# Performance work log

Measured on AMD Instinct MI355X. Metric: run time of the kernel, lower is better.

The kernel has to match this reference:

```python
import jax, jax.numpy as jnp
import numpy as np

D_MODEL = 4096
N_Q_HEAD = 32
N_KV_HEAD = 8
HEAD_DIM = D_MODEL // N_Q_HEAD  # 128
N_REP = N_Q_HEAD // N_KV_HEAD   # 4
B, T = 2, 2048


def _rope_tables(seq_len, head_dim, dtype=jnp.float32):
    # theta_i = 10000^(-2*(i-1)/d) for i=1..d/2  (matches torch.pow(10000, -2*(arange(1,d/2+1)-1)/d))
    i = jnp.arange(head_dim // 2, dtype=dtype)
    theta = jnp.power(10000.0, -2.0 * i / head_dim)
    angles = jnp.outer(jnp.arange(seq_len, dtype=dtype), theta)  # [T, d/2]
    return jnp.cos(angles), jnp.sin(angles)


def _apply_rope(x, cos, sin):
    # x: [B, T, h, HD]; pairs are consecutive elements (view_as_complex semantics)
    B_, T_, h, hd = x.shape
    xp = x.reshape(B_, T_, h, hd // 2, 2)
    xr, xi = xp[..., 0], xp[..., 1]
    c = cos[None, :T_, None, :]
    s = sin[None, :T_, None, :]
    out_r = xr * c - xi * s
    out_i = xr * s + xi * c
    return jnp.stack([out_r, out_i], axis=-1).reshape(B_, T_, h, hd)


def setup_inputs() -> dict:
    key = jax.random.key(0)
    ks = jax.random.split(key, 5)
    scale = 0.02
    x = jax.random.normal(ks[0], (B, T, D_MODEL), dtype=jnp.float32)
    wq = jax.random.normal(ks[1], (D_MODEL, N_Q_HEAD * HEAD_DIM), dtype=jnp.float32) * scale
    wk = jax.random.normal(ks[2], (D_MODEL, N_KV_HEAD * HEAD_DIM), dtype=jnp.float32) * scale
    wv = jax.random.normal(ks[3], (D_MODEL, N_KV_HEAD * HEAD_DIM), dtype=jnp.float32) * scale
    wo = jax.random.normal(ks[4], (N_Q_HEAD * HEAD_DIM, D_MODEL), dtype=jnp.float32) * scale
    # causal mask: 1 where masked (strict upper triangle), per masked_fill(mask==1, -inf)
    attention_mask = jnp.triu(jnp.ones((T, T), dtype=jnp.int32), k=1)
    return {"x": x, "wq": wq, "wk": wk, "wv": wv, "wo": wo, "attention_mask": attention_mask}


def reference(x, wq, wk, wv, wo, attention_mask):
    B_, T_, _ = x.shape
    xq = (x @ wq).reshape(B_, T_, N_Q_HEAD, HEAD_DIM)
    xk = (x @ wk).reshape(B_, T_, N_KV_HEAD, HEAD_DIM)
    xv = (x @ wv).reshape(B_, T_, N_KV_HEAD, HEAD_DIM)

    cos, sin = _rope_tables(T_, HEAD_DIM, x.dtype)
    xq = _apply_rope(xq, cos, sin)
    xk = _apply_rope(xk, cos, sin)

    # GQA: repeat kv heads (training path: no cache)
    xk = jnp.repeat(xk, N_REP, axis=2)  # [B, T, HQ, HD]
    xv = jnp.repeat(xv, N_REP, axis=2)

    q = xq.transpose(0, 2, 1, 3)  # [B, H, T, HD]
    k = xk.transpose(0, 2, 1, 3)
    v = xv.transpose(0, 2, 1, 3)

    scores = jnp.einsum('bhqd,bhkd->bhqk', q, k) / jnp.sqrt(jnp.asarray(HEAD_DIM, x.dtype))
    scores = jnp.where(attention_mask[None, None, :, :] == 1, -jnp.inf, scores)
    probs = jax.nn.softmax(scores, axis=-1)
    out = jnp.einsum('bhqk,bhkd->bhqd', probs, v)
    out = out.transpose(0, 2, 1, 3).reshape(B_, T_, N_Q_HEAD * HEAD_DIM)
    return out @ wo
```

## Files before the change

### kernel.cpp

```cpp
#include <hip/hip_runtime.h>
#include <hip/hip_bf16.h>
#include <math.h>

typedef __hip_bfloat16 bf16;
typedef short bf16x8 __attribute__((ext_vector_type(8)));
typedef float f32x4 __attribute__((ext_vector_type(4)));
typedef float f32x16 __attribute__((ext_vector_type(16)));
typedef unsigned int u32;
typedef unsigned short u16;

#define GLD16(g, l)                                                            \
  __builtin_amdgcn_global_load_lds(                                            \
      (const __attribute__((address_space(1))) void*)(g),                      \
      (__attribute__((address_space(3))) void*)(l), 16, 0, 0)

#define SBAR() __builtin_amdgcn_s_barrier()
#define VMCNT(n) asm volatile("s_waitcnt vmcnt(" #n ")")
#define LGKM0() asm volatile("s_waitcnt lgkmcnt(0)")

__global__ void convert_f32_bf16(const float* __restrict__ in,
                                 bf16* __restrict__ out) {
  size_t i = ((size_t)blockIdx.x * 256 + threadIdx.x) * 4;
  float4 v = *(const float4*)(in + i);
  out[i + 0] = __float2bfloat16(v.x);
  out[i + 1] = __float2bfloat16(v.y);
  out[i + 2] = __float2bfloat16(v.z);
  out[i + 3] = __float2bfloat16(v.w);
}

__global__ void transpose_f32_bf16(const float* __restrict__ in,
                                   bf16* __restrict__ out, int R, int C) {
  __shared__ bf16 tile[32][33];
  int tx = threadIdx.x & 31, ty = threadIdx.x >> 5;
  int c0 = blockIdx.x * 32, r0 = blockIdx.y * 32;
#pragma unroll
  for (int i = 0; i < 32; i += 8)
    tile[ty + i][tx] = __float2bfloat16(in[(size_t)(r0 + ty + i) * C + c0 + tx]);
  __syncthreads();
#pragma unroll
  for (int i = 0; i < 32; i += 8)
    out[(size_t)(c0 + ty + i) * R + r0 + tx] = tile[tx][ty + i];
}

__global__ void transpose_v(const bf16* __restrict__ V, bf16* __restrict__ VT) {
  __shared__ bf16 tile[32][33];
  int s = blockIdx.z, b = s >> 3, kvh = s & 7;
  int t0 = blockIdx.x * 32, d0 = blockIdx.y * 32;
  int tx = threadIdx.x & 31, ty = threadIdx.x >> 5;
#pragma unroll
  for (int i = 0; i < 32; i += 8)
    tile[ty + i][tx] =
        V[(size_t)(b * 2048 + t0 + ty + i) * 6144 + kvh * 128 + d0 + tx];
  __syncthreads();
#pragma unroll
  for (int i = 0; i < 32; i += 8)
    VT[((size_t)s * 128 + d0 + ty + i) * 2048 + t0 + tx] = tile[tx][ty + i];
}

__global__ void rope_table_k(float* __restrict__ tab) {
  int idx = blockIdx.x * 256 + threadIdx.x;
  int t = idx >> 6, i = idx & 63;
  float theta = powf(10000.0f, -2.0f * (float)i / 128.0f);
  float ang = (float)t * theta;
  tab[idx * 2 + 0] = cosf(ang);
  tab[idx * 2 + 1] = sinf(ang);
}

__global__ void rope_apply(bf16* __restrict__ X, const float* __restrict__ tab,
                           int nheads, int rowstride, float omul) {
  size_t idx = (size_t)blockIdx.x * 256 + threadIdx.x;
  int i = (int)(idx & 63);
  size_t rest = idx >> 6;
  int h = (int)(rest % nheads);
  size_t r = rest / nheads;
  int t = (int)(r & 2047);
  float c = tab[(t * 64 + i) * 2 + 0];
  float s = tab[(t * 64 + i) * 2 + 1];
  bf16* p = X + r * (size_t)rowstride + h * 128 + 2 * i;
  float xr = __bfloat162float(p[0]), xi = __bfloat162float(p[1]);
  p[0] = __float2bfloat16((xr * c - xi * s) * omul);
  p[1] = __float2bfloat16((xr * s + xi * c) * omul);
}

template <typename OutT>
__global__ __launch_bounds__(512, 2) void gemm_bt8(const bf16* __restrict__ A,
                                                   const bf16* __restrict__ BT,
                                                   OutT* __restrict__ C, int M,
                                                   int N, int K) {
  __shared__ bf16 AS[2][2][128 * 64];
  __shared__ bf16 BS[2][2][128 * 64];

  const int tid = threadIdx.x;
  const int lane = tid & 63;
  const int w = tid >> 6, wm = w >> 2, wn = w & 3;
  const int lr = lane & 15, hi = lane >> 4;

  int gx = gridDim.x;
  int nwg = gx * gridDim.y;
  int bid = blockIdx.y * gx + blockIdx.x;
  int swz = (bid & 7) * (nwg >> 3) + (bid >> 3);
  const int m0 = (swz / gx) * 256, n0 = (swz % gx) * 256;

  const int NKT = K >> 6;
  const int NI = K >> 7;
  const int srow = tid >> 3;
  const int scol = ((tid & 7) ^ (srow & 7)) << 3;

  f32x4 acc[8][4];
#pragma unroll
  for (int m = 0; m < 8; ++m)
#pragma unroll
    for (int n = 0; n < 4; ++n)
#pragma unroll
      for (int j = 0; j < 4; ++j) acc[m][n][j] = 0.f;

  auto STAGE_A = [&](int buf, int kt) {
    int kk0 = (kt < NKT) ? kt * 64 : 0;
#pragma unroll
    for (int hs = 0; hs < 4; ++hs) {
      int ha = hs >> 1, sa = hs & 1;
      const bf16* g = A + (size_t)(m0 + ha * 128 + sa * 64 + srow) * K + kk0 + scol;
      GLD16(g, &AS[buf][ha][(sa * 64 + srow) * 64 + (tid & 7) * 8]);
    }
  };
  auto STAGE_B = [&](int buf, int kt, int half) {
    int kk0 = (kt < NKT) ? kt * 64 : 0;
#pragma unroll
    for (int sa = 0; sa < 2; ++sa) {
      const bf16* g =
          BT + (size_t)(n0 + half * 128 + sa * 64 + srow) * K + kk0 + scol;
      GLD16(g, &BS[buf][half][(sa * 64 + srow) * 64 + (tid & 7) * 8]);
    }
  };

  bf16x8 bfr[4][2], afA[2][2], afB[2][2];
  auto READ_B = [&](int buf) {
#pragma unroll
    for (int n = 0; n < 4; ++n) {
      int row = (wn & 1) * 64 + n * 16 + lr;
#pragma unroll
      for (int kk = 0; kk < 2; ++kk)
        bfr[n][kk] = *(const bf16x8*)(&BS[buf][wn >> 1]
                                         [row * 64 + (((kk * 4 + hi) ^ (row & 7)) << 3)]);
    }
  };
  auto READ_A_TO = [&](bf16x8(&dst)[2][2], int buf, int q) {
#pragma unroll
    for (int mm = 0; mm < 2; ++mm) {
      int row = (q * 2 + mm) * 16 + lr;
#pragma unroll
      for (int kk = 0; kk < 2; ++kk)
        dst[mm][kk] = *(const bf16x8*)(&AS[buf][wm]
                                          [row * 64 + (((kk * 4 + hi) ^ (row & 7)) << 3)]);
    }
  };

#define MFMA16(q, AF)                                                          \
  do {                                                                         \
    _Pragma("unroll") for (int mm = 0; mm < 2; ++mm)                           \
        _Pragma("unroll") for (int n = 0; n < 4; ++n)                          \
        _Pragma("unroll") for (int kk = 0; kk < 2; ++kk)                       \
            acc[(q) * 2 + mm][n] = __builtin_amdgcn_mfma_f32_16x16x32_bf16(    \
                AF[mm][kk], bfr[n][kk], acc[(q) * 2 + mm][n], 0, 0, 0);        \
  } while (0)

  STAGE_A(0, 0);
  STAGE_B(0, 0, 0); STAGE_B(0, 0, 1);
  STAGE_B(1, 1, 0); STAGE_B(1, 1, 1);
  VMCNT(4);
  SBAR();

  for (int i = 0; i < NI; ++i) {
    int t = 2 * i;
    READ_B(0); READ_A_TO(afA, 0, 0); READ_A_TO(afB, 0, 1);
    STAGE_A(1, t + 1);
    SBAR(); LGKM0();
    __builtin_amdgcn_s_setprio(1); MFMA16(0, afA); MFMA16(1, afB);
    __builtin_amdgcn_s_setprio(0);
    SBAR();
    READ_A_TO(afA, 0, 2); READ_A_TO(afB, 0, 3);
    STAGE_B(0, t + 2, 0); STAGE_B(0, t + 2, 1);
    SBAR(); LGKM0();
    __builtin_amdgcn_s_setprio(1); MFMA16(2, afA); MFMA16(3, afB);
    __builtin_amdgcn_s_setprio(0);
    VMCNT(4);
    SBAR();
    READ_B(1); READ_A_TO(afA, 1, 0); READ_A_TO(afB, 1, 1);
    STAGE_A(0, t + 2);
    SBAR(); LGKM0();
    __builtin_amdgcn_s_setprio(1); MFMA16(0, afA); MFMA16(1, afB);
    __builtin_amdgcn_s_setprio(0);
    SBAR();
    READ_A_TO(afA, 1, 2); READ_A_TO(afB, 1, 3);
    STAGE_B(1, t + 3, 0); STAGE_B(1, t + 3, 1);
    SBAR(); LGKM0();
    __builtin_amdgcn_s_setprio(1); MFMA16(2, afA); MFMA16(3, afB);
    __builtin_amdgcn_s_setprio(0);
    VMCNT(4);
    SBAR();
  }

  VMCNT(0);
  SBAR();

#pragma unroll
  for (int m = 0; m < 8; ++m) {
    int row_base = m0 + wm * 128 + m * 16 + hi * 4;
#pragma unroll
    for (int n = 0; n < 4; ++n) {
      int col = n0 + wn * 64 + n * 16 + lr;
#pragma unroll
      for (int j = 0; j < 4; ++j) {
        float v = acc[m][n][j];
        if constexpr (sizeof(OutT) == 2)
          C[(size_t)(row_base + j) * N + col] = (OutT)__float2bfloat16(v);
        else
          C[(size_t)(row_base + j) * N + col] = (OutT)v;
      }
    }
  }
#undef MFMA16
}

static __device__ inline u32 cvtpk_bf16(float a, float b) {
  u32 r;
  asm("v_cvt_pk_bf16_f32 %0, %1, %2" : "=v"(r) : "v"(a), "v"(b));
  return r;
}

__global__ __launch_bounds__(256) void flash_attn3(const bf16* __restrict__ Q,
                                                   const bf16* __restrict__ K,
                                                   const bf16* __restrict__ VT,
                                                   const float* __restrict__ tab,
                                                   bf16* __restrict__ AO) {
  __shared__ bf16 Kbuf[2][64 * 128];
  __shared__ bf16 Vbuf[2][128 * 64];

  int bid = blockIdx.x;
  int lid = (bid & 7) * 128 + (bid >> 3);
  int qt = 15 - (lid & 15);
  int hq = (lid >> 4) & 3;
  int kvh = (lid >> 6) & 7;
  int b = lid >> 9;
  int h = kvh * 4 + hq;

  const int tid = threadIdx.x;
  const int lane = tid & 63, w = tid >> 6;
  const int ql = lane & 31, hi = lane >> 5;
  const int qrow0 = qt * 128 + w * 32;
  const int nt = 2 * qt + 2;

  const bf16* Kg0 = K + (size_t)b * 2048 * 6144 + kvh * 128;
  const bf16* Vg0 = VT + (size_t)(b * 8 + kvh) * 128 * 2048;

  bf16x8 qf[8];
  {
    int tpos = qrow0 + ql;
    const bf16* qb = Q + (size_t)(b * 2048 + tpos) * 6144 + h * 128 + hi * 8;
    const float* tb = tab + (size_t)tpos * 128;
    const float QS = 1.4426950408889634f * 0.08838834764831845f;
#pragma unroll
    for (int dc = 0; dc < 8; ++dc) {
      union { bf16x8 v; u16 s[8]; } in;
      in.v = *(const bf16x8*)(qb + dc * 16);
      union { u32 u[4]; bf16x8 v; } o;
#pragma unroll
      for (int p = 0; p < 4; ++p) {
        int ii = dc * 8 + hi * 4 + p;
        float2 cs = *(const float2*)(tb + 2 * ii);
        float xr = __uint_as_float((u32)in.s[2 * p] << 16);
        float xi = __uint_as_float((u32)in.s[2 * p + 1] << 16);
        o.u[p] = cvtpk_bf16((xr * cs.x - xi * cs.y) * QS,
                            (xr * cs.y + xi * cs.x) * QS);
      }
      qf[dc] = o.v;
    }
  }

  f32x16 O[4];
#pragma unroll
  for (int d4 = 0; d4 < 4; ++d4)
#pragma unroll
    for (int e = 0; e < 16; ++e) O[d4][e] = 0.f;
  float m_ = -1e30f, l_ = 0.f;

  auto STAGE = [&](int buf, int kv0) {
    bf16* Ks = &Kbuf[buf][0];
    bf16* Vs = &Vbuf[buf][0];
    const bf16* Kg = Kg0 + (size_t)kv0 * 6144;
    const bf16* Vg = Vg0 + kv0;
#pragma unroll
    for (int it = 0; it < 4; ++it) {
      int s = it * 256 + tid;
      int row = s >> 4, c = s & 15;
      GLD16(Kg + (size_t)row * 6144 + ((c ^ (row & 7)) << 3), Ks + s * 8);
    }
#pragma unroll
    for (int it = 0; it < 4; ++it) {
      int s = it * 256 + tid;
      int row = s >> 3, c = s & 7;
      GLD16(Vg + (size_t)row * 2048 + ((c ^ (row & 7)) << 3), Vs + s * 8);
    }
  };

  STAGE(0, 0);
  __syncthreads();

  for (int t = 0; t < nt; ++t) {
    int kv0 = t * 64;
    if (t + 1 < nt) STAGE((t + 1) & 1, kv0 + 64);

    if (kv0 <= qrow0 + 31) {
      const bf16* Ks = &Kbuf[t & 1][0];
      const bf16* Vs = &Vbuf[t & 1][0];

      f32x16 Sx[2];
#pragma unroll
      for (int cb = 0; cb < 2; ++cb)
#pragma unroll
        for (int e = 0; e < 16; ++e) Sx[cb][e] = 0.f;

      __builtin_amdgcn_s_setprio(1);
#pragma unroll
      for (int cb = 0; cb < 2; ++cb) {
        int krow = cb * 32 + ql;
#pragma unroll
        for (int dc = 0; dc < 8; ++dc) {
          bf16x8 kf = *(const bf16x8*)(Ks + krow * 128 +
                                       (((dc * 2 + hi) ^ (ql & 7)) << 3));
          Sx[cb] = __builtin_amdgcn_mfma_f32_32x32x16_bf16(kf, qf[dc], Sx[cb],
                                                           0, 0, 0);
        }
      }
      __builtin_amdgcn_s_setprio(0);

      int q = qrow0 + ql;
      bool domask = (kv0 + 63 > qrow0);
      if (domask) {
#pragma unroll
        for (int cb = 0; cb < 2; ++cb)
#pragma unroll
          for (int r = 0; r < 16; ++r) {
            int kv = kv0 + cb * 32 + (r & 3) + 8 * (r >> 2) + 4 * hi;
            if (kv > q) Sx[cb][r] = -1e30f;
          }
      }
      float x0 = -1e30f, x1 = -1e30f, x2 = -1e30f, x3 = -1e30f;
#pragma unroll
      for (int cb = 0; cb < 2; ++cb)
#pragma unroll
        for (int r = 0; r < 16; r += 4) {
          x0 = fmaxf(x0, Sx[cb][r + 0]);
          x1 = fmaxf(x1, Sx[cb][r + 1]);
          x2 = fmaxf(x2, Sx[cb][r + 2]);
          x3 = fmaxf(x3, Sx[cb][r + 3]);
        }
      float pm = fmaxf(fmaxf(x0, x1), fmaxf(x2, x3));
      pm = fmaxf(pm, __shfl_xor(pm, 32));

      if (!__all(pm - m_ <= 11.5416f)) {
        float nm = fmaxf(m_, pm);
        float rs = exp2f(m_ - nm);
        m_ = nm;
        l_ *= rs;
#pragma unroll
        for (int d4 = 0; d4 < 4; ++d4)
#pragma unroll
          for (int e = 0; e < 16; ++e) O[d4][e] *= rs;
      }
      float s0 = 0.f, s1 = 0.f, s2 = 0.f, s3 = 0.f;
#pragma unroll
      for (int cb = 0; cb < 2; ++cb)
#pragma unroll
        for (int r = 0; r < 16; r += 4) {
          float p0 = exp2f(Sx[cb][r + 0] - m_);
          float p1 = exp2f(Sx[cb][r + 1] - m_);
          float p2 = exp2f(Sx[cb][r + 2] - m_);
          float p3 = exp2f(Sx[cb][r + 3] - m_);
          Sx[cb][r + 0] = p0; Sx[cb][r + 1] = p1;
          Sx[cb][r + 2] = p2; Sx[cb][r + 3] = p3;
          s0 += p0; s1 += p1; s2 += p2; s3 += p3;
        }
      float ps = (s0 + s1) + (s2 + s3);
      ps += __shfl_xor(ps, 32);
      l_ += ps;

      bf16x8 pb[4];
#pragma unroll
      for (int kb = 0; kb < 4; ++kb) {
        int cb = kb >> 1, r0 = 8 * (kb & 1);
        u32 Av = cvtpk_bf16(Sx[cb][r0 + 0], Sx[cb][r0 + 1]);
        u32 Bv = cvtpk_bf16(Sx[cb][r0 + 2], Sx[cb][r0 + 3]);
        u32 Cv = cvtpk_bf16(Sx[cb][r0 + 4], Sx[cb][r0 + 5]);
        u32 Dv = cvtpk_bf16(Sx[cb][r0 + 6], Sx[cb][r0 + 7]);
        u32 sA = (u32)__shfl_xor((int)Av, 32);
        u32 sB = (u32)__shfl_xor((int)Bv, 32);
        u32 sC = (u32)__shfl_xor((int)Cv, 32);
        u32 sD = (u32)__shfl_xor((int)Dv, 32);
        union { u32 u[4]; bf16x8 v; } pk;
        pk.u[0] = hi ? sC : Av;
        pk.u[1] = hi ? sD : Bv;
        pk.u[2] = hi ? Cv : sA;
        pk.u[3] = hi ? Dv : sB;
        pb[kb] = pk.v;
      }

      __builtin_amdgcn_s_setprio(1);
#pragma unroll
      for (int d4 = 0; d4 < 4; ++d4) {
        int vrow = d4 * 32 + ql;
#pragma unroll
        for (int kb = 0; kb < 4; ++kb) {
          bf16x8 vf = *(const bf16x8*)(Vs + vrow * 64 +
                                       (((kb * 2 + hi) ^ (ql & 7)) << 3));
          O[d4] = __builtin_amdgcn_mfma_f32_32x32x16_bf16(vf, pb[kb], O[d4], 0,
                                                          0, 0);
        }
      }
      __builtin_amdgcn_s_setprio(0);
    }
    __syncthreads();
  }

  float inv = 1.0f / l_;
  bf16* outp = AO + (size_t)(b * 2048 + qrow0 + ql) * 4096 + h * 128;
#pragma unroll
  for (int d4 = 0; d4 < 4; ++d4)
#pragma unroll
    for (int rg = 0; rg < 4; ++rg) {
      union { u16 s[4]; unsigned long long v; } pk;
#pragma unroll
      for (int j = 0; j < 4; ++j)
        pk.s[j] = __bfloat16_as_ushort(__float2bfloat16(O[d4][rg * 4 + j] * inv));
      *(unsigned long long*)(outp + d4 * 32 + rg * 8 + hi * 4) = pk.v;
    }
}

extern "C" void kernel_launch(void* const* d_in, const int* in_sizes, int n_in,
                              void* d_out, int out_size, void* d_ws,
                              size_t ws_size, hipStream_t stream) {
  const float* x = (const float*)d_in[0];
  const float* wq = (const float*)d_in[1];
  const float* wk = (const float*)d_in[2];
  const float* wv = (const float*)d_in[3];
  const float* wo = (const float*)d_in[4];

  char* ws = (char*)d_ws;
  bf16* xb    = (bf16*)(ws + 0);
  bf16* WqkvT = (bf16*)(ws + 33554432);
  bf16* WoT   = (bf16*)(ws + 83886080);
  bf16* QKV   = (bf16*)(ws + 117440512);
  bf16* VTb   = (bf16*)(ws + 167772160);
  float* tab  = (float*)(ws + 176160768);
  bf16* AOb   = xb;

  convert_f32_bf16<<<16384, 256, 0, stream>>>(x, xb);
  transpose_f32_bf16<<<dim3(128, 128), 256, 0, stream>>>(wq, WqkvT, 4096, 4096);
  transpose_f32_bf16<<<dim3(32, 128), 256, 0, stream>>>(
      wk, WqkvT + (size_t)4096 * 4096, 4096, 1024);
  transpose_f32_bf16<<<dim3(32, 128), 256, 0, stream>>>(
      wv, WqkvT + (size_t)5120 * 4096, 4096, 1024);
  transpose_f32_bf16<<<dim3(128, 128), 256, 0, stream>>>(wo, WoT, 4096, 4096);
  rope_table_k<<<512, 256, 0, stream>>>(tab);

  gemm_bt8<bf16><<<dim3(24, 16), 512, 0, stream>>>(xb, WqkvT, QKV, 4096, 6144,
                                                   4096);

  rope_apply<<<8192, 256, 0, stream>>>(QKV + 4096, tab, 8, 6144, 1.0f);

  transpose_v<<<dim3(64, 4, 16), 256, 0, stream>>>(QKV + 5120, VTb);

  flash_attn3<<<1024, 256, 0, stream>>>(QKV, QKV + 4096, VTb, tab, AOb);

  gemm_bt8<float><<<dim3(16, 16), 512, 0, stream>>>(AOb, WoT, (float*)d_out,
                                                    4096, 4096, 4096);
}
```

Before: 652.0 us.

## Double query rows per warp in flash attention to reuse K/V fragments

Each warp now handles two 32-row query sub-tiles (64 rows, 256 per block), so every K and V fragment read from LDS feeds two MFMAs. The grid is halved to 512 blocks and the block-to-tile mapping is reordered so kv heads are interleaved across consecutive blocks. The aim is to cut LDS traffic and global K/V staging per query row. In exchange, register pressure roughly doubles (launch_bounds min 1 block), there are fewer blocks for load balance across the causal triangle, and masking waste on diagonal tiles grows.

```diff
diff --git a/kernel.cpp b/kernel.cpp
--- a/kernel.cpp
+++ b/kernel.cpp
@@ -228,34 +228,35 @@
   return r;
 }
 
-__global__ __launch_bounds__(256) void flash_attn3(const bf16* __restrict__ Q,
-                                                   const bf16* __restrict__ K,
-                                                   const bf16* __restrict__ VT,
-                                                   const float* __restrict__ tab,
-                                                   bf16* __restrict__ AO) {
+__global__ __launch_bounds__(256, 1) void flash_attn3(const bf16* __restrict__ Q,
+                                                      const bf16* __restrict__ K,
+                                                      const bf16* __restrict__ VT,
+                                                      const float* __restrict__ tab,
+                                                      bf16* __restrict__ AO) {
   __shared__ bf16 Kbuf[2][64 * 128];
   __shared__ bf16 Vbuf[2][128 * 64];
 
   int bid = blockIdx.x;
-  int lid = (bid & 7) * 128 + (bid >> 3);
-  int qt = 15 - (lid & 15);
-  int hq = (lid >> 4) & 3;
-  int kvh = (lid >> 6) & 7;
-  int b = lid >> 9;
+  int b = bid >> 8;
+  int i = (bid >> 3) & 31;
+  int kvh = bid & 7;
+  int hq = i >> 3;
+  int qt = 7 - (i & 7);
   int h = kvh * 4 + hq;
 
   const int tid = threadIdx.x;
   const int lane = tid & 63, w = tid >> 6;
   const int ql = lane & 31, hi = lane >> 5;
-  const int qrow0 = qt * 128 + w * 32;
-  const int nt = 2 * qt + 2;
+  const int qrow0 = qt * 256 + w * 64;
+  const int nt = 4 * qt + 4;
 
   const bf16* Kg0 = K + (size_t)b * 2048 * 6144 + kvh * 128;
   const bf16* Vg0 = VT + (size_t)(b * 8 + kvh) * 128 * 2048;
 
-  bf16x8 qf[8];
-  {
-    int tpos = qrow0 + ql;
+  bf16x8 qf[2][8];
+#pragma unroll
+  for (int mi = 0; mi < 2; ++mi) {
+    int tpos = qrow0 + mi * 32 + ql;
     const bf16* qb = Q + (size_t)(b * 2048 + tpos) * 6144 + h * 128 + hi * 8;
     const float* tb = tab + (size_t)tpos * 128;
     const float QS = 1.4426950408889634f * 0.08838834764831845f;
@@ -273,16 +274,21 @@
         o.u[p] = cvtpk_bf16((xr * cs.x - xi * cs.y) * QS,
                             (xr * cs.y + xi * cs.x) * QS);
       }
-      qf[dc] = o.v;
-    }
-  }
-
-  f32x16 O[4];
-#pragma unroll
-  for (int d4 = 0; d4 < 4; ++d4)
-#pragma unroll
-    for (int e = 0; e < 16; ++e) O[d4][e] = 0.f;
-  float m_ = -1e30f, l_ = 0.f;
+      qf[mi][dc] = o.v;
+    }
+  }
+
+  f32x16 O[2][4];
+  float m_[2], l_[2];
+#pragma unroll
+  for (int mi = 0; mi < 2; ++mi) {
+    m_[mi] = -1e30f;
+    l_[mi] = 0.f;
+#pragma unroll
+    for (int d4 = 0; d4 < 4; ++d4)
+#pragma unroll
+      for (int e = 0; e < 16; ++e) O[mi][d4][e] = 0.f;
+  }
 
   auto STAGE = [&](int buf, int kv0) {
     bf16* Ks = &Kbuf[buf][0];
@@ -310,15 +316,17 @@
     int kv0 = t * 64;
     if (t + 1 < nt) STAGE((t + 1) & 1, kv0 + 64);
 
-    if (kv0 <= qrow0 + 31) {
+    if (kv0 <= qrow0 + 63) {
       const bf16* Ks = &Kbuf[t & 1][0];
       const bf16* Vs = &Vbuf[t & 1][0];
 
-      f32x16 Sx[2];
-#pragma unroll
-      for (int cb = 0; cb < 2; ++cb)
-#pragma unroll
-        for (int e = 0; e < 16; ++e) Sx[cb][e] = 0.f;
+      f32x16 Sx[2][2];
+#pragma unroll
+      for (int mi = 0; mi < 2; ++mi)
+#pragma unroll
+        for (int cb = 0; cb < 2; ++cb)
+#pragma unroll
+          for (int e = 0; e < 16; ++e) Sx[mi][cb][e] = 0.f;
 
       __builtin_amdgcn_s_setprio(1);
 #pragma unroll
@@ -328,81 +336,85 @@
         for (int dc = 0; dc < 8; ++dc) {
           bf16x8 kf = *(const bf16x8*)(Ks + krow * 128 +
                                        (((dc * 2 + hi) ^ (ql & 7)) << 3));
-          Sx[cb] = __builtin_amdgcn_mfma_f32_32x32x16_bf16(kf, qf[dc], Sx[cb],
-                                                           0, 0, 0);
+          Sx[0][cb] = __builtin_amdgcn_mfma_f32_32x32x16_bf16(kf, qf[0][dc],
+                                                              Sx[0][cb], 0, 0, 0);
+          Sx[1][cb] = __builtin_amdgcn_mfma_f32_32x32x16_bf16(kf, qf[1][dc],
+                                                              Sx[1][cb], 0, 0, 0);
         }
       }
       __builtin_amdgcn_s_setprio(0);
 
-      int q = qrow0 + ql;
-      bool domask = (kv0 + 63 > qrow0);
-      if (domask) {
+      bf16x8 pb[2][4];
+#pragma unroll
+      for (int mi = 0; mi < 2; ++mi) {
+        int q = qrow0 + mi * 32 + ql;
+        if (kv0 + 63 > qrow0 + mi * 32) {
+#pragma unroll
+          for (int cb = 0; cb < 2; ++cb)
+#pragma unroll
+            for (int r = 0; r < 16; ++r) {
+              int kv = kv0 + cb * 32 + (r & 3) + 8 * (r >> 2) + 4 * hi;
+              if (kv > q) Sx[mi][cb][r] = -1e30f;
+            }
+        }
+        float x0 = -1e30f, x1 = -1e30f, x2 = -1e30f, x3 = -1e30f;
 #pragma unroll
         for (int cb = 0; cb < 2; ++cb)
 #pragma unroll
-          for (int r = 0; r < 16; ++r) {
-            int kv = kv0 + cb * 32 + (r & 3) + 8 * (r >> 2) + 4 * hi;
-            if (kv > q) Sx[cb][r] = -1e30f;
+          for (int r = 0; r < 16; r += 4) {
+            x0 = fmaxf(x0, Sx[mi][cb][r + 0]);
+            x1 = fmaxf(x1, Sx[mi][cb][r + 1]);
+            x2 = fmaxf(x2, Sx[mi][cb][r + 2]);
+            x3 = fmaxf(x3, Sx[mi][cb][r + 3]);
           }
-      }
-      float x0 = -1e30f, x1 = -1e30f, x2 = -1e30f, x3 = -1e30f;
-#pragma unroll
-      for (int cb = 0; cb < 2; ++cb)
-#pragma unroll
-        for (int r = 0; r < 16; r += 4) {
-          x0 = fmaxf(x0, Sx[cb][r + 0]);
-          x1 = fmaxf(x1, Sx[cb][r + 1]);
-          x2 = fmaxf(x2, Sx[cb][r + 2]);
-          x3 = fmaxf(x3, Sx[cb][r + 3]);
+        float pm = fmaxf(fmaxf(x0, x1), fmaxf(x2, x3));
+        pm = fmaxf(pm, __shfl_xor(pm, 32));
+
+        if (!__all(pm - m_[mi] <= 11.5416f)) {
+          float nm = fmaxf(m_[mi], pm);
+          float rs = exp2f(m_[mi] - nm);
+          m_[mi] = nm;
+          l_[mi] *= rs;
+#pragma unroll
+          for (int d4 = 0; d4 < 4; ++d4)
+#pragma unroll
+            for (int e = 0; e < 16; ++e) O[mi][d4][e] *= rs;
         }
-      float pm = fmaxf(fmaxf(x0, x1), fmaxf(x2, x3));
-      pm = fmaxf(pm, __shfl_xor(pm, 32));
-
-      if (!__all(pm - m_ <= 11.5416f)) {
-        float nm = fmaxf(m_, pm);
-        float rs = exp2f(m_ - nm);
-        m_ = nm;
-        l_ *= rs;
-#pragma unroll
-        for (int d4 = 0; d4 < 4; ++d4)
-#pragma unroll
-          for (int e = 0; e < 16; ++e) O[d4][e] *= rs;
-      }
-      float s0 = 0.f, s1 = 0.f, s2 = 0.f, s3 = 0.f;
-#pragma unroll
-      for (int cb = 0; cb < 2; ++cb)
-#pragma unroll
-        for (int r = 0; r < 16; r += 4) {
-          float p0 = exp2f(Sx[cb][r + 0] - m_);
-          float p1 = exp2f(Sx[cb][r + 1] - m_);
-          float p2 = exp2f(Sx[cb][r + 2] - m_);
-          float p3 = exp2f(Sx[cb][r + 3] - m_);
-          Sx[cb][r + 0] = p0; Sx[cb][r + 1] = p1;
-          Sx[cb][r + 2] = p2; Sx[cb][r + 3] = p3;
-          s0 += p0; s1 += p1; s2 += p2; s3 += p3;
+        float s0 = 0.f, s1 = 0.f, s2 = 0.f, s3 = 0.f;
+#pragma unroll
+        for (int cb = 0; cb < 2; ++cb)
+#pragma unroll
+          for (int r = 0; r < 16; r += 4) {
+            float p0 = exp2f(Sx[mi][cb][r + 0] - m_[mi]);
+            float p1 = exp2f(Sx[mi][cb][r + 1] - m_[mi]);
+            float p2 = exp2f(Sx[mi][cb][r + 2] - m_[mi]);
+            float p3 = exp2f(Sx[mi][cb][r + 3] - m_[mi]);
+            Sx[mi][cb][r + 0] = p0; Sx[mi][cb][r + 1] = p1;
+            Sx[mi][cb][r + 2] = p2; Sx[mi][cb][r + 3] = p3;
+            s0 += p0; s1 += p1; s2 += p2; s3 += p3;
+          }
+        float ps = (s0 + s1) + (s2 + s3);
+        ps += __shfl_xor(ps, 32);
+        l_[mi] += ps;
+
+#pragma unroll
+        for (int kb = 0; kb < 4; ++kb) {
+          int cb = kb >> 1, r0 = 8 * (kb & 1);
+          u32 Av = cvtpk_bf16(Sx[mi][cb][r0 + 0], Sx[mi][cb][r0 + 1]);
+          u32 Bv = cvtpk_bf16(Sx[mi][cb][r0 + 2], Sx[mi][cb][r0 + 3]);
+          u32 Cv = cvtpk_bf16(Sx[mi][cb][r0 + 4], Sx[mi][cb][r0 + 5]);
+          u32 Dv = cvtpk_bf16(Sx[mi][cb][r0 + 6], Sx[mi][cb][r0 + 7]);
+          u32 sA = (u32)__shfl_xor((int)Av, 32);
+          u32 sB = (u32)__shfl_xor((int)Bv, 32);
+          u32 sC = (u32)__shfl_xor((int)Cv, 32);
+          u32 sD = (u32)__shfl_xor((int)Dv, 32);
+          union { u32 u[4]; bf16x8 v; } pk;
+          pk.u[0] = hi ? sC : Av;
+          pk.u[1] = hi ? sD : Bv;
+          pk.u[2] = hi ? Cv : sA;
+          pk.u[3] = hi ? Dv : sB;
+          pb[mi][kb] = pk.v;
         }
-      float ps = (s0 + s1) + (s2 + s3);
-      ps += __shfl_xor(ps, 32);
-      l_ += ps;
-
-      bf16x8 pb[4];
-#pragma unroll
-      for (int kb = 0; kb < 4; ++kb) {
-        int cb = kb >> 1, r0 = 8 * (kb & 1);
-        u32 Av = cvtpk_bf16(Sx[cb][r0 + 0], Sx[cb][r0 + 1]);
-        u32 Bv = cvtpk_bf16(Sx[cb][r0 + 2], Sx[cb][r0 + 3]);
-        u32 Cv = cvtpk_bf16(Sx[cb][r0 + 4], Sx[cb][r0 + 5]);
-        u32 Dv = cvtpk_bf16(Sx[cb][r0 + 6], Sx[cb][r0 + 7]);
-        u32 sA = (u32)__shfl_xor((int)Av, 32);
-        u32 sB = (u32)__shfl_xor((int)Bv, 32);
-        u32 sC = (u32)__shfl_xor((int)Cv, 32);
-        u32 sD = (u32)__shfl_xor((int)Dv, 32);
-        union { u32 u[4]; bf16x8 v; } pk;
-        pk.u[0] = hi ? sC : Av;
-        pk.u[1] = hi ? sD : Bv;
-        pk.u[2] = hi ? Cv : sA;
-        pk.u[3] = hi ? Dv : sB;
-        pb[kb] = pk.v;
       }
 
       __builtin_amdgcn_s_setprio(1);
@@ -413,8 +425,10 @@
         for (int kb = 0; kb < 4; ++kb) {
           bf16x8 vf = *(const bf16x8*)(Vs + vrow * 64 +
                                        (((kb * 2 + hi) ^ (ql & 7)) << 3));
-          O[d4] = __builtin_amdgcn_mfma_f32_32x32x16_bf16(vf, pb[kb], O[d4], 0,
-                                                          0, 0);
+          O[0][d4] = __builtin_amdgcn_mfma_f32_32x32x16_bf16(vf, pb[0][kb],
+                                                             O[0][d4], 0, 0, 0);
+          O[1][d4] = __builtin_amdgcn_mfma_f32_32x32x16_bf16(vf, pb[1][kb],
+                                                             O[1][d4], 0, 0, 0);
         }
       }
       __builtin_amdgcn_s_setprio(0);
@@ -422,18 +436,23 @@
     __syncthreads();
   }
 
-  float inv = 1.0f / l_;
-  bf16* outp = AO + (size_t)(b * 2048 + qrow0 + ql) * 4096 + h * 128;
-#pragma unroll
-  for (int d4 = 0; d4 < 4; ++d4)
-#pragma unroll
-    for (int rg = 0; rg < 4; ++rg) {
-      union { u16 s[4]; unsigned long long v; } pk;
-#pragma unroll
-      for (int j = 0; j < 4; ++j)
-        pk.s[j] = __bfloat16_as_ushort(__float2bfloat16(O[d4][rg * 4 + j] * inv));
-      *(unsigned long long*)(outp + d4 * 32 + rg * 8 + hi * 4) = pk.v;
-    }
+#pragma unroll
+  for (int mi = 0; mi < 2; ++mi) {
+    float inv = 1.0f / l_[mi];
+    bf16* outp =
+        AO + (size_t)(b * 2048 + qrow0 + mi * 32 + ql) * 4096 + h * 128;
+#pragma unroll
+    for (int d4 = 0; d4 < 4; ++d4)
+#pragma unroll
+      for (int rg = 0; rg < 4; ++rg) {
+        union { u16 s[4]; unsigned long long v; } pk;
+#pragma unroll
+        for (int j = 0; j < 4; ++j)
+          pk.s[j] =
+              __bfloat16_as_ushort(__float2bfloat16(O[mi][d4][rg * 4 + j] * inv));
+        *(unsigned long long*)(outp + d4 * 32 + rg * 8 + hi * 4) = pk.v;
+      }
+  }
 }
 
 extern "C" void kernel_launch(void* const* d_in, const int* in_sizes, int n_in,
@@ -470,7 +489,7 @@
 
   transpose_v<<<dim3(64, 4, 16), 256, 0, stream>>>(QKV + 5120, VTb);
 
-  flash_attn3<<<1024, 256, 0, stream>>>(QKV, QKV + 4096, VTb, tab, AOb);
+  flash_attn3<<<512, 256, 0, stream>>>(QKV, QKV + 4096, VTb, tab, AOb);
 
   gemm_bt8<float><<<dim3(16, 16), 512, 0, stream>>>(AOb, WoT, (float*)d_out,
                                                     4096, 4096, 4096);
```

Measured after the change: 697.6 us. 7.0% more time.
